# Kernel tuning notes

Hardware: AMD Instinct MI355X
Metric: run time of the kernel (lower is better)

The kernel has to match this reference:

```python
import jax, jax.numpy as jnp
import numpy as np

B, S, D = 4, 4096, 1024
H, K = 16, 64            # num_heads, intermediate_dim
DV = 1024                # vector_dim
FINAL = H * K            # 1024
EPS_ATT = 1e-30
EPS_LN = 1e-6


def setup_inputs() -> dict:
    key = jax.random.key(0)
    ks = jax.random.split(key, 12)
    s = 0.02
    return {
        "inputs": jax.random.normal(ks[0], (B, S, D), jnp.float32),
        "vector": jax.random.normal(ks[1], (B, DV), jnp.float32),
        "attention_weights": jax.random.normal(ks[2], (D, H), jnp.float32) * s,
        "temperature": jnp.ones((1, 1, H), jnp.float32),
        "values": jax.random.normal(ks[3], (D, H, K), jnp.float32) * s,
        "operator": jax.random.normal(ks[4], (FINAL, DV), jnp.float32) * s,
        "ff1": jax.random.normal(ks[5], (DV + D, D), jnp.float32) * s,
        "ff1_bias": jnp.zeros((1, 1, D), jnp.float32),
        "ff2": jax.random.normal(ks[6], (D, D), jnp.float32) * s,
        "ff2_bias": jnp.zeros((1, 1, D), jnp.float32),
        "ln_gamma": jnp.ones((D,), jnp.float32),
        "ln_beta": jnp.zeros((D,), jnp.float32),
    }


def reference(inputs, vector, attention_weights, temperature, values, operator,
              ff1, ff1_bias, ff2, ff2_bias, ln_gamma, ln_beta):
    # att[b,q,h]: per-query head weight (constant over keys in the original code)
    att = inputs @ attention_weights                      # (B,S,H)
    att = att - jnp.max(att, axis=1, keepdims=True)
    att = jnp.exp(att * temperature)                      # temperature (1,1,H)

    # values per position, then causal prefix sum over keys.
    # Original: sum_{s<=q} att[b,q,h]*v[b,s,h,k] / (sum_{s<=q} att[b,q,h] + 1e-30)
    v = jnp.einsum('bsi,ihk->bshk', inputs, values)       # (B,S,H,K)
    cumv = jnp.cumsum(v, axis=1)                          # (B,S,H,K)
    counts = jnp.arange(1, S + 1, dtype=inputs.dtype)[None, :, None]  # (1,S,1)
    denom = att * counts + EPS_ATT                        # (B,S,H)
    attn_out = (att[..., None] * cumv) / denom[..., None]  # (B,S,H,K)
    attn_out = attn_out.reshape(attn_out.shape[0], S, FINAL)

    op = attn_out @ operator + vector[:, None, :]         # (B,S,DV)
    concat = jnp.concatenate([inputs, op], axis=-1)       # (B,S,D+DV)
    res = jax.nn.relu(concat @ ff1 + ff1_bias)
    res = res @ ff2 + ff2_bias + inputs

    # LayerNorm (keras, eps=1e-6, last axis)
    mu = jnp.mean(res, axis=-1, keepdims=True)
    var = jnp.mean(jnp.square(res - mu), axis=-1, keepdims=True)
    xhat = (res - mu) * jax.lax.rsqrt(var + EPS_LN)
    return xhat * ln_gamma + ln_beta
```

## Files before the change

kernel.cpp:

```cpp
#include <hip/hip_runtime.h>
#include <math.h>

#define BB 4
#define SS 4096
#define DD 1024
#define DVV 1024
#define CHUNK 128
#define NCHUNK (SS/CHUNK)

typedef unsigned short u16;
typedef __bf16 bf16x8 __attribute__((ext_vector_type(8)));
typedef float f32x4 __attribute__((ext_vector_type(4)));
#define AS1 __attribute__((address_space(1)))
#define AS3 __attribute__((address_space(3)))

__device__ __forceinline__ u16 f2bf(float f) {
    union { float f; unsigned u; } v; v.f = f;
    unsigned r = (v.u + 0x7fffu + ((v.u >> 16) & 1u)) >> 16;
    return (u16)r;
}
__device__ __forceinline__ float bf2f(u16 h) {
    union { unsigned u; float f; } v; v.u = ((unsigned)h) << 16;
    return v.f;
}

__device__ __forceinline__ void transp_sec(const float* __restrict__ src, int src_ld,
                                           u16* __restrict__ dst, int dst_ld, int koff,
                                           int tb, float* sm) {
    int k0 = (tb & 31) * 32, n0 = (tb >> 5) * 32;
    int tx = threadIdx.x & 31, ty = threadIdx.x >> 5;
    #pragma unroll
    for (int i = 0; i < 32; i += 8)
        sm[(ty + i) * 33 + tx] = src[(size_t)(k0 + ty + i) * src_ld + n0 + tx];
    __syncthreads();
    #pragma unroll
    for (int i = 0; i < 32; i += 8)
        dst[(size_t)(n0 + ty + i) * dst_ld + koff + k0 + tx] = f2bf(sm[tx * 33 + ty + i]);
}

__global__ __launch_bounds__(256) void prep_k(const float* __restrict__ X,
                                              const float* __restrict__ vec,
                                              const float* __restrict__ values,
                                              const float* __restrict__ oper,
                                              const float* __restrict__ ff1,
                                              const float* __restrict__ ff1b,
                                              const float* __restrict__ ff2,
                                              u16* __restrict__ Vbf,
                                              u16* __restrict__ OpT,
                                              u16* __restrict__ FbT,
                                              u16* __restrict__ Bt1,
                                              u16* __restrict__ Bt2,
                                              float* __restrict__ csum,
                                              float* __restrict__ bias2) {
    __shared__ float sm[1056];
    int bid = blockIdx.x;
    int t = threadIdx.x;
    if (bid < 1024) {
        int g = bid * 256 + t;
        float4 v = *(const float4*)&values[(size_t)g * 4];
        u16* o = Vbf + (size_t)g * 4;
        o[0] = f2bf(v.x); o[1] = f2bf(v.y); o[2] = f2bf(v.z); o[3] = f2bf(v.w);
    } else if (bid < 2048) {
        transp_sec(oper, DD, OpT, 1024, 0, bid - 1024, sm);
    } else if (bid < 3072) {
        transp_sec(ff1 + (size_t)DD * DD, DD, FbT, 1024, 0, bid - 2048, sm);
    } else if (bid < 4096) {
        transp_sec(ff1, DD, Bt1, 2048, 0, bid - 3072, sm);
    } else if (bid < 5120) {
        transp_sec(ff2, DD, Bt2, 1024, 0, bid - 4096, sm);
    } else if (bid < 5632) {
        int g = (bid - 5120) * 256 + t;
        int d = g & (DD - 1);
        int c = (g >> 10) & (NCHUNK - 1);
        int b = g >> 15;
        const float* p = X + ((size_t)(b * SS + c * CHUNK)) * DD + d;
        float s = 0.f;
        for (int tt = 0; tt < CHUNK; ++tt) s += p[(size_t)tt * DD];
        csum[g] = s;
    } else {
        int j0 = (bid - 5632) * 32;
        int j = t & 31, g = t >> 5;
        const float* fb = ff1 + (size_t)DD * DD;
        float s[4] = {0.f, 0.f, 0.f, 0.f};
        for (int dv = g * 128; dv < g * 128 + 128; ++dv) {
            float w = fb[(size_t)dv * DD + j0 + j];
            s[0] += vec[dv] * w;
            s[1] += vec[DVV + dv] * w;
            s[2] += vec[2 * DVV + dv] * w;
            s[3] += vec[3 * DVV + dv] * w;
        }
        #pragma unroll
        for (int b = 0; b < 4; ++b) sm[g * 128 + b * 32 + j] = s[b];
        __syncthreads();
        if (t < 128) {
            int jj = t & 31, b = t >> 5;
            float acc = ff1b[j0 + jj];
            #pragma unroll
            for (int gg = 0; gg < 8; ++gg) acc += sm[gg * 128 + b * 32 + jj];
            bias2[b * DD + j0 + jj] = acc;
        }
    }
}

__global__ void chunk_prefix_k(float* csum) {
    int g = blockIdx.x * 256 + threadIdx.x;
    int d = g & (DD - 1);
    int b = g >> 10;
    float* p = csum + ((size_t)b * NCHUNK) * DD + d;
    float run = 0.f;
    for (int c = 0; c < NCHUNK; ++c) {
        float v = p[(size_t)c * DD];
        p[(size_t)c * DD] = run;
        run += v;
    }
}

__global__ void write_mean_conv_k(const float* __restrict__ X, const float* __restrict__ csum,
                                  u16* __restrict__ Xbf, u16* __restrict__ Mbf) {
    int g = blockIdx.x * 256 + threadIdx.x;
    int d = (g & 511) * 2;
    int c = (g >> 9) & (NCHUNK - 1);
    int b = g >> 14;
    size_t cs = ((size_t)(b * NCHUNK + c)) * DD + d;
    float run0 = csum[cs], run1 = csum[cs + 1];
    size_t base = ((size_t)(b * SS + c * CHUNK)) * DD + d;
    const float* p = X + base;
    u16* qx = Xbf + base;
    u16* qm = Mbf + base;
    int s0 = c * CHUNK;
    for (int t = 0; t < CHUNK; ++t) {
        float2 x = *(const float2*)&p[(size_t)t * DD];
        run0 += x.x; run1 += x.y;
        float inv = 1.0f / (float)(s0 + t + 1);
        u16 h0 = f2bf(x.x), h1 = f2bf(x.y);
        u16 m0 = f2bf(run0 * inv), m1 = f2bf(run1 * inv);
        *(ushort2*)&qx[(size_t)t * DD] = make_ushort2(h0, h1);
        *(ushort2*)&qm[(size_t)t * DD] = make_ushort2(m0, m1);
    }
}

__global__ __launch_bounds__(256) void mfma64_k(const u16* __restrict__ Ag,
                                                const u16* __restrict__ Btg,
                                                u16* __restrict__ dst, int K,
                                                int dld, int koff) {
    __shared__ u16 Alds[64 * 32];
    __shared__ u16 Blds[64 * 32];
    f32x4 acc[2][2] = {};
    int bm = blockIdx.y * 64, bn = blockIdx.x * 64;
    const int tid = threadIdx.x;
    const int wave = tid >> 6, lane = tid & 63;
    const int wm = wave & 1, wn = wave >> 1;
    const u16* ga = Ag + (size_t)(bm + (tid >> 2)) * K + (tid & 3) * 8;
    const u16* gb = Btg + (size_t)(bn + (tid >> 2)) * K + (tid & 3) * 8;
    const int lo = tid * 8;
    const int fk = (lane >> 4) * 8;
    for (int kt = 0; kt < K; kt += 32) {
        __builtin_amdgcn_global_load_lds((const AS1 void*)(ga + kt), (AS3 void*)(Alds + lo), 16, 0, 0);
        __builtin_amdgcn_global_load_lds((const AS1 void*)(gb + kt), (AS3 void*)(Blds + lo), 16, 0, 0);
        __syncthreads();
        bf16x8 af[2], bfr[2];
        #pragma unroll
        for (int i = 0; i < 2; ++i) af[i] = *(const bf16x8*)&Alds[(wm * 32 + i * 16 + (lane & 15)) * 32 + fk];
        #pragma unroll
        for (int i = 0; i < 2; ++i) bfr[i] = *(const bf16x8*)&Blds[(wn * 32 + i * 16 + (lane & 15)) * 32 + fk];
        #pragma unroll
        for (int mi = 0; mi < 2; ++mi)
            #pragma unroll
            for (int ni = 0; ni < 2; ++ni)
                acc[mi][ni] = __builtin_amdgcn_mfma_f32_16x16x32_bf16(af[mi], bfr[ni], acc[mi][ni], 0, 0, 0);
        __syncthreads();
    }
    #pragma unroll
    for (int mi = 0; mi < 2; ++mi)
        #pragma unroll
        for (int ni = 0; ni < 2; ++ni) {
            int col = bn + wn * 32 + ni * 16 + (lane & 15);
            #pragma unroll
            for (int r = 0; r < 4; ++r) {
                int row = bm + wm * 32 + mi * 16 + (lane >> 4) * 4 + r;
                dst[(size_t)row * dld + koff + col] = f2bf(acc[mi][ni][r]);
            }
        }
}

__device__ __forceinline__ void mfma_core(const u16* __restrict__ Ag, int lda,
                                          const u16* __restrict__ Btg, int ldb,
                                          int K, int bm, int bn,
                                          u16* Alds, u16* Blds, f32x4 acc[4][4]) {
    const int tid = threadIdx.x;
    const int wave = tid >> 6, lane = tid & 63;
    const int lrow = lane >> 2;
    const int lkb = (lane & 3) * 8;
    const int s0 = wave * 2;
    const u16* ga0 = Ag + (size_t)(bm + s0 * 16 + lrow) * lda + lkb;
    const u16* ga1 = Ag + (size_t)(bm + s0 * 16 + 16 + lrow) * lda + lkb;
    const u16* gb0 = Btg + (size_t)(bn + s0 * 16 + lrow) * ldb + lkb;
    const u16* gb1 = Btg + (size_t)(bn + s0 * 16 + 16 + lrow) * ldb + lkb;
    const int lo0 = s0 * 512;
    const int lo1 = lo0 + 512;
    const int fm = (wave & 1) * 64 + (lane & 15);
    const int fn = (wave >> 1) * 64 + (lane & 15);
    const int fk = (lane >> 4) * 8;
    for (int kt = 0; kt < K; kt += 32) {
        __builtin_amdgcn_global_load_lds((const AS1 void*)(ga0 + kt), (AS3 void*)(Alds + lo0), 16, 0, 0);
        __builtin_amdgcn_global_load_lds((const AS1 void*)(ga1 + kt), (AS3 void*)(Alds + lo1), 16, 0, 0);
        __builtin_amdgcn_global_load_lds((const AS1 void*)(gb0 + kt), (AS3 void*)(Blds + lo0), 16, 0, 0);
        __builtin_amdgcn_global_load_lds((const AS1 void*)(gb1 + kt), (AS3 void*)(Blds + lo1), 16, 0, 0);
        __syncthreads();
        bf16x8 af[4], bfr[4];
        #pragma unroll
        for (int i = 0; i < 4; ++i) af[i] = *(const bf16x8*)&Alds[(fm + i * 16) * 32 + fk];
        #pragma unroll
        for (int i = 0; i < 4; ++i) bfr[i] = *(const bf16x8*)&Blds[(fn + i * 16) * 32 + fk];
        #pragma unroll
        for (int mi = 0; mi < 4; ++mi)
            #pragma unroll
            for (int ni = 0; ni < 4; ++ni)
                acc[mi][ni] = __builtin_amdgcn_mfma_f32_16x16x32_bf16(af[mi], bfr[ni], acc[mi][ni], 0, 0, 0);
        __syncthreads();
    }
}

__device__ __forceinline__ void swizzle_mn(int nblk_n, int& bm, int& bn) {
    int bid = blockIdx.y * nblk_n + blockIdx.x;
    int x = bid & 7;
    int j = bid >> 3;
    int nt = j & (nblk_n - 1);
    int mt = (j >> 3) * 8 + x;
    bm = mt * 128;
    bn = nt * 128;
}

__global__ __launch_bounds__(256) void mfma_ff1_k(const u16* __restrict__ Xbf,
                                                  const u16* __restrict__ Mbf,
                                                  const u16* __restrict__ Bt1,
                                                  const float* __restrict__ bias2,
                                                  u16* __restrict__ H) {
    __shared__ u16 Alds[128 * 32];
    __shared__ u16 Blds[128 * 32];
    f32x4 acc[4][4] = {};
    int bm, bn;
    swizzle_mn(8, bm, bn);
    mfma_core(Xbf, 1024, Bt1, 2048, 1024, bm, bn, Alds, Blds, acc);
    mfma_core(Mbf, 1024, Bt1 + 1024, 2048, 1024, bm, bn, Alds, Blds, acc);
    int wave = threadIdx.x >> 6, lane = threadIdx.x & 63;
    int rbase = bm + (wave & 1) * 64 + (lane >> 4) * 4;
    int cbase = bn + (wave >> 1) * 64 + (lane & 15);
    int bb = bm >> 12;
    #pragma unroll
    for (int mi = 0; mi < 4; ++mi)
        #pragma unroll
        for (int ni = 0; ni < 4; ++ni) {
            int col = cbase + ni * 16;
            float bz = bias2[bb * 1024 + col];
            #pragma unroll
            for (int r = 0; r < 4; ++r) {
                int row = rbase + mi * 16 + r;
                float v = acc[mi][ni][r] + bz;
                H[(size_t)row * 1024 + col] = f2bf(fmaxf(v, 0.f));
            }
        }
}

__global__ __launch_bounds__(256) void mfma_ff2_k(const u16* __restrict__ H,
                                                  const u16* __restrict__ Bt2,
                                                  const float* __restrict__ ff2b,
                                                  const u16* __restrict__ Xbf,
                                                  u16* __restrict__ P) {
    __shared__ u16 Alds[128 * 32];
    __shared__ u16 Blds[128 * 32];
    f32x4 acc[4][4] = {};
    int bm, bn;
    swizzle_mn(8, bm, bn);
    mfma_core(H, 1024, Bt2, 1024, 1024, bm, bn, Alds, Blds, acc);
    int wave = threadIdx.x >> 6, lane = threadIdx.x & 63;
    int rbase = bm + (wave & 1) * 64 + (lane >> 4) * 4;
    int cbase = bn + (wave >> 1) * 64 + (lane & 15);
    #pragma unroll
    for (int mi = 0; mi < 4; ++mi)
        #pragma unroll
        for (int ni = 0; ni < 4; ++ni) {
            int col = cbase + ni * 16;
            float bz = ff2b[col];
            #pragma unroll
            for (int r = 0; r < 4; ++r) {
                int row = rbase + mi * 16 + r;
                float xr = bf2f(Xbf[(size_t)row * 1024 + col]);
                P[(size_t)row * 1024 + col] = f2bf(acc[mi][ni][r] + bz + xr);
            }
        }
}

__global__ __launch_bounds__(256) void ln_k(const u16* __restrict__ P,
                                            const float* __restrict__ gam,
                                            const float* __restrict__ bet,
                                            float* __restrict__ out) {
    __shared__ float sbuf[4];
    int row = blockIdx.x;
    int tid = threadIdx.x;
    const u16* pr = P + (size_t)row * DD + tid * 4;
    float x0 = bf2f(pr[0]), x1 = bf2f(pr[1]), x2 = bf2f(pr[2]), x3 = bf2f(pr[3]);
    float local = x0 + x1 + x2 + x3;
    #pragma unroll
    for (int o = 32; o > 0; o >>= 1) local += __shfl_down(local, o, 64);
    if ((tid & 63) == 0) sbuf[tid >> 6] = local;
    __syncthreads();
    float mu = (sbuf[0] + sbuf[1] + sbuf[2] + sbuf[3]) * (1.0f / 1024.0f);
    __syncthreads();
    float d0 = x0 - mu, d1 = x1 - mu, d2 = x2 - mu, d3 = x3 - mu;
    float v2 = d0 * d0 + d1 * d1 + d2 * d2 + d3 * d3;
    #pragma unroll
    for (int o = 32; o > 0; o >>= 1) v2 += __shfl_down(v2, o, 64);
    if ((tid & 63) == 0) sbuf[tid >> 6] = v2;
    __syncthreads();
    float var = (sbuf[0] + sbuf[1] + sbuf[2] + sbuf[3]) * (1.0f / 1024.0f);
    float rs = rsqrtf(var + 1e-6f);
    float4 gg = *(const float4*)&gam[tid * 4];
    float4 bb = *(const float4*)&bet[tid * 4];
    float4 o4;
    o4.x = d0 * rs * gg.x + bb.x;
    o4.y = d1 * rs * gg.y + bb.y;
    o4.z = d2 * rs * gg.z + bb.z;
    o4.w = d3 * rs * gg.w + bb.w;
    *(float4*)&out[(size_t)row * DD + tid * 4] = o4;
}

extern "C" void kernel_launch(void* const* d_in, const int* in_sizes, int n_in,
                              void* d_out, int out_size, void* d_ws, size_t ws_size,
                              hipStream_t stream) {
    const float* X      = (const float*)d_in[0];
    const float* vec    = (const float*)d_in[1];
    const float* values = (const float*)d_in[4];
    const float* oper   = (const float*)d_in[5];
    const float* ff1    = (const float*)d_in[6];
    const float* ff1b   = (const float*)d_in[7];
    const float* ff2    = (const float*)d_in[8];
    const float* ff2b   = (const float*)d_in[9];
    const float* gam    = (const float*)d_in[10];
    const float* bet    = (const float*)d_in[11];
    float* out = (float*)d_out;

    char* w = (char*)d_ws;
    u16*   Xbf   = (u16*)w;
    u16*   Mbf   = (u16*)(w + (size_t)(32u << 20));
    u16*   Pbf   = Mbf;
    u16*   Hbf   = (u16*)(w + (size_t)(64u << 20));
    u16*   Vbf   = (u16*)(w + (size_t)(96u << 20));
    u16*   OpT   = (u16*)(w + (size_t)(98u << 20));
    u16*   FbT   = (u16*)(w + (size_t)(100u << 20));
    u16*   WvBf  = (u16*)(w + (size_t)(102u << 20));
    u16*   Bt1   = (u16*)(w + (size_t)(104u << 20));
    u16*   Bt2   = (u16*)(w + (size_t)(108u << 20));
    float* bias2 = (float*)(w + (size_t)(110u << 20));
    float* csum  = (float*)(w + (size_t)(110u << 20) + (1u << 16));

    prep_k<<<5664, 256, 0, stream>>>(X, vec, values, oper, ff1, ff1b, ff2,
                                     Vbf, OpT, FbT, Bt1, Bt2, csum, bias2);

    mfma64_k<<<dim3(16, 16), 256, 0, stream>>>(Vbf, OpT, WvBf, 1024, 1024, 0);
    mfma64_k<<<dim3(16, 16), 256, 0, stream>>>(FbT, WvBf, Bt1, 1024, 2048, 1024);

    chunk_prefix_k<<<16, 256, 0, stream>>>(csum);
    write_mean_conv_k<<<256, 256, 0, stream>>>(X, csum, Xbf, Mbf);

    mfma_ff1_k<<<dim3(8, 128), 256, 0, stream>>>(Xbf, Mbf, Bt1, bias2, Hbf);
    mfma_ff2_k<<<dim3(8, 128), 256, 0, stream>>>(Hbf, Bt2, ff2b, Xbf, Pbf);

    ln_k<<<BB * SS, 256, 0, stream>>>(Pbf, gam, bet, out);
}
```

Baseline: 366.8 us.

## Merge independent small kernels into combined launches and interleave X/mean into one A matrix

New measurement: 352.5 us. 3.9% less time.

```diff
diff --git a/kernel.cpp b/kernel.cpp
--- a/kernel.cpp
+++ b/kernel.cpp
@@ -102,51 +102,13 @@
     }
 }
 
-__global__ void chunk_prefix_k(float* csum) {
-    int g = blockIdx.x * 256 + threadIdx.x;
-    int d = g & (DD - 1);
-    int b = g >> 10;
-    float* p = csum + ((size_t)b * NCHUNK) * DD + d;
-    float run = 0.f;
-    for (int c = 0; c < NCHUNK; ++c) {
-        float v = p[(size_t)c * DD];
-        p[(size_t)c * DD] = run;
-        run += v;
-    }
-}
-
-__global__ void write_mean_conv_k(const float* __restrict__ X, const float* __restrict__ csum,
-                                  u16* __restrict__ Xbf, u16* __restrict__ Mbf) {
-    int g = blockIdx.x * 256 + threadIdx.x;
-    int d = (g & 511) * 2;
-    int c = (g >> 9) & (NCHUNK - 1);
-    int b = g >> 14;
-    size_t cs = ((size_t)(b * NCHUNK + c)) * DD + d;
-    float run0 = csum[cs], run1 = csum[cs + 1];
-    size_t base = ((size_t)(b * SS + c * CHUNK)) * DD + d;
-    const float* p = X + base;
-    u16* qx = Xbf + base;
-    u16* qm = Mbf + base;
-    int s0 = c * CHUNK;
-    for (int t = 0; t < CHUNK; ++t) {
-        float2 x = *(const float2*)&p[(size_t)t * DD];
-        run0 += x.x; run1 += x.y;
-        float inv = 1.0f / (float)(s0 + t + 1);
-        u16 h0 = f2bf(x.x), h1 = f2bf(x.y);
-        u16 m0 = f2bf(run0 * inv), m1 = f2bf(run1 * inv);
-        *(ushort2*)&qx[(size_t)t * DD] = make_ushort2(h0, h1);
-        *(ushort2*)&qm[(size_t)t * DD] = make_ushort2(m0, m1);
-    }
-}
-
-__global__ __launch_bounds__(256) void mfma64_k(const u16* __restrict__ Ag,
-                                                const u16* __restrict__ Btg,
-                                                u16* __restrict__ dst, int K,
-                                                int dld, int koff) {
+__device__ __forceinline__ void mfma64_dev(const u16* __restrict__ Ag,
+                                           const u16* __restrict__ Btg,
+                                           u16* __restrict__ dst, int K,
+                                           int dld, int koff, int bm, int bn) {
     __shared__ u16 Alds[64 * 32];
     __shared__ u16 Blds[64 * 32];
     f32x4 acc[2][2] = {};
-    int bm = blockIdx.y * 64, bn = blockIdx.x * 64;
     const int tid = threadIdx.x;
     const int wave = tid >> 6, lane = tid & 63;
     const int wm = wave & 1, wn = wave >> 1;
@@ -181,6 +143,58 @@
                 dst[(size_t)row * dld + koff + col] = f2bf(acc[mi][ni][r]);
             }
         }
+}
+
+__global__ __launch_bounds__(256) void k2_k(float* __restrict__ csum,
+                                            const u16* __restrict__ Vbf,
+                                            const u16* __restrict__ OpT,
+                                            u16* __restrict__ WvBf) {
+    int bid = blockIdx.x;
+    if (bid < 16) {
+        int g = bid * 256 + threadIdx.x;
+        int d = g & (DD - 1);
+        int b = g >> 10;
+        float* p = csum + ((size_t)b * NCHUNK) * DD + d;
+        float run = 0.f;
+        for (int c = 0; c < NCHUNK; ++c) {
+            float v = p[(size_t)c * DD];
+            p[(size_t)c * DD] = run;
+            run += v;
+        }
+    } else {
+        int t2 = bid - 16;
+        mfma64_dev(Vbf, OpT, WvBf, 1024, 1024, 0, (t2 >> 4) * 64, (t2 & 15) * 64);
+    }
+}
+
+__global__ __launch_bounds__(256) void k3_k(const float* __restrict__ X,
+                                            const float* __restrict__ csum,
+                                            u16* __restrict__ Acat,
+                                            const u16* __restrict__ FbT,
+                                            const u16* __restrict__ WvBf,
+                                            u16* __restrict__ Bt1) {
+    int bid = blockIdx.x;
+    if (bid < 256) {
+        int g = bid * 256 + threadIdx.x;
+        int d = (g & 511) * 2;
+        int c = (g >> 9) & (NCHUNK - 1);
+        int b = g >> 14;
+        size_t cs = ((size_t)(b * NCHUNK + c)) * DD + d;
+        float run0 = csum[cs], run1 = csum[cs + 1];
+        const float* p = X + ((size_t)(b * SS + c * CHUNK)) * DD + d;
+        u16* q = Acat + ((size_t)(b * SS + c * CHUNK)) * 2048 + d;
+        int s0 = c * CHUNK;
+        for (int t = 0; t < CHUNK; ++t) {
+            float2 x = *(const float2*)&p[(size_t)t * DD];
+            run0 += x.x; run1 += x.y;
+            float inv = 1.0f / (float)(s0 + t + 1);
+            *(ushort2*)&q[(size_t)t * 2048] = make_ushort2(f2bf(x.x), f2bf(x.y));
+            *(ushort2*)&q[(size_t)t * 2048 + 1024] = make_ushort2(f2bf(run0 * inv), f2bf(run1 * inv));
+        }
+    } else {
+        int t2 = bid - 256;
+        mfma64_dev(FbT, WvBf, Bt1, 1024, 2048, 1024, (t2 >> 4) * 64, (t2 & 15) * 64);
+    }
 }
 
 __device__ __forceinline__ void mfma_core(const u16* __restrict__ Ag, int lda,
@@ -231,8 +245,7 @@
     bn = nt * 128;
 }
 
-__global__ __launch_bounds__(256) void mfma_ff1_k(const u16* __restrict__ Xbf,
-                                                  const u16* __restrict__ Mbf,
+__global__ __launch_bounds__(256) void mfma_ff1_k(const u16* __restrict__ Acat,
                                                   const u16* __restrict__ Bt1,
                                                   const float* __restrict__ bias2,
                                                   u16* __restrict__ H) {
@@ -241,8 +254,7 @@
     f32x4 acc[4][4] = {};
     int bm, bn;
     swizzle_mn(8, bm, bn);
-    mfma_core(Xbf, 1024, Bt1, 2048, 1024, bm, bn, Alds, Blds, acc);
-    mfma_core(Mbf, 1024, Bt1 + 1024, 2048, 1024, bm, bn, Alds, Blds, acc);
+    mfma_core(Acat, 2048, Bt1, 2048, 2048, bm, bn, Alds, Blds, acc);
     int wave = threadIdx.x >> 6, lane = threadIdx.x & 63;
     int rbase = bm + (wave & 1) * 64 + (lane >> 4) * 4;
     int cbase = bn + (wave >> 1) * 64 + (lane & 15);
@@ -265,7 +277,7 @@
 __global__ __launch_bounds__(256) void mfma_ff2_k(const u16* __restrict__ H,
                                                   const u16* __restrict__ Bt2,
                                                   const float* __restrict__ ff2b,
-                                                  const u16* __restrict__ Xbf,
+                                                  const float* __restrict__ X,
                                                   u16* __restrict__ P) {
     __shared__ u16 Alds[128 * 32];
     __shared__ u16 Blds[128 * 32];
@@ -285,8 +297,7 @@
             #pragma unroll
             for (int r = 0; r < 4; ++r) {
                 int row = rbase + mi * 16 + r;
-                float xr = bf2f(Xbf[(size_t)row * 1024 + col]);
-                P[(size_t)row * 1024 + col] = f2bf(acc[mi][ni][r] + bz + xr);
+                P[(size_t)row * 1024 + col] = f2bf(acc[mi][ni][r] + bz + X[(size_t)row * 1024 + col]);
             }
         }
 }
@@ -341,9 +352,8 @@
     float* out = (float*)d_out;
 
     char* w = (char*)d_ws;
-    u16*   Xbf   = (u16*)w;
-    u16*   Mbf   = (u16*)(w + (size_t)(32u << 20));
-    u16*   Pbf   = Mbf;
+    u16*   Acat  = (u16*)w;
+    u16*   Pbf   = (u16*)w;
     u16*   Hbf   = (u16*)(w + (size_t)(64u << 20));
     u16*   Vbf   = (u16*)(w + (size_t)(96u << 20));
     u16*   OpT   = (u16*)(w + (size_t)(98u << 20));
@@ -356,15 +366,9 @@
 
     prep_k<<<5664, 256, 0, stream>>>(X, vec, values, oper, ff1, ff1b, ff2,
                                      Vbf, OpT, FbT, Bt1, Bt2, csum, bias2);
-
-    mfma64_k<<<dim3(16, 16), 256, 0, stream>>>(Vbf, OpT, WvBf, 1024, 1024, 0);
-    mfma64_k<<<dim3(16, 16), 256, 0, stream>>>(FbT, WvBf, Bt1, 1024, 2048, 1024);
-
-    chunk_prefix_k<<<16, 256, 0, stream>>>(csum);
-    write_mean_conv_k<<<256, 256, 0, stream>>>(X, csum, Xbf, Mbf);
-
-    mfma_ff1_k<<<dim3(8, 128), 256, 0, stream>>>(Xbf, Mbf, Bt1, bias2, Hbf);
-    mfma_ff2_k<<<dim3(8, 128), 256, 0, stream>>>(Hbf, Bt2, ff2b, Xbf, Pbf);
-
+    k2_k<<<272, 256, 0, stream>>>(csum, Vbf, OpT, WvBf);
+    k3_k<<<512, 256, 0, stream>>>(X, csum, Acat, FbT, WvBf, Bt1);
+    mfma_ff1_k<<<dim3(8, 128), 256, 0, stream>>>(Acat, Bt1, bias2, Hbf);
+    mfma_ff2_k<<<dim3(8, 128), 256, 0, stream>>>(Hbf, Bt2, ff2b, X, Pbf);
     ln_k<<<BB * SS, 256, 0, stream>>>(Pbf, gam, bet, out);
 }
```
